# Kernel optimization log

Hardware: AMD Instinct MI355X
Metric: run time of the kernel (lower is better)

Reference implementation:

```python
import jax, jax.numpy as jnp
import numpy as np

NUM_NODES = 100000
EMB_DIM = 64
NUM_EDGES = 1280000
NUM_LAYERS = 3


def setup_inputs() -> dict:
    key = jax.random.key(0)
    k1, k2 = jax.random.split(key)
    edge_index = jax.random.randint(k1, (2, NUM_EDGES), 0, NUM_NODES, dtype=jnp.int32)
    emb = jax.random.normal(k2, (NUM_NODES, EMB_DIM), dtype=jnp.float32) * 0.01
    return {"edge_index": edge_index, "emb": emb}


def _lgconv_norm(edge_index):
    # PyG gcn_norm without self-loops: deg over destination nodes,
    # norm_e = deg[src]^-0.5 * deg[dst]^-0.5
    src, dst = edge_index[0], edge_index[1]
    deg = jax.ops.segment_sum(jnp.ones((edge_index.shape[1],), jnp.float32), dst,
                              num_segments=NUM_NODES)
    dinv = jnp.where(deg > 0, jax.lax.rsqrt(jnp.maximum(deg, 1.0)), 0.0)
    return src, dst, dinv[src] * dinv[dst]


def reference(edge_index, emb):
    src, dst, w = _lgconv_norm(edge_index)
    x = emb
    out = x
    for _ in range(NUM_LAYERS):
        # message: gather source embeddings, scale, scatter-add to destination
        x = jax.ops.segment_sum(x[src] * w[:, None], dst, num_segments=NUM_NODES)
        out = out + x
    return out / (NUM_LAYERS + 1)
```

## Files before the change

kernel.cpp:

```cpp
#include <hip/hip_runtime.h>

#define N_NODES 100000
#define EMB 64
#define N_EDGES 1280000
#define N_E4 (N_EDGES / 4)

#define NBUCK 196
#define BUCK_SHIFT 9
#define BUCK_NODES 512
#define NBA 313
#define HTOT (NBUCK * NBA)
#define NBH ((HTOT + 1023) / 1024)

typedef unsigned long long u64;
typedef _Float16 f16;
typedef __attribute__((ext_vector_type(2))) _Float16 f16x2;

__global__ void bucket_hist_kernel(const int* __restrict__ dst, int* __restrict__ hist) {
    __shared__ int lh[NBUCK];
    for (int i = threadIdx.x; i < NBUCK; i += 256) lh[i] = 0;
    __syncthreads();
#pragma unroll
    for (int k = 0; k < 4; ++k) {
        int q = blockIdx.x * 1024 + k * 256 + threadIdx.x;
        if (q < N_E4) {
            int4 d4 = ((const int4*)dst)[q];
            atomicAdd(&lh[d4.x >> BUCK_SHIFT], 1);
            atomicAdd(&lh[d4.y >> BUCK_SHIFT], 1);
            atomicAdd(&lh[d4.z >> BUCK_SHIFT], 1);
            atomicAdd(&lh[d4.w >> BUCK_SHIFT], 1);
        }
    }
    __syncthreads();
    for (int i = threadIdx.x; i < NBUCK; i += 256)
        hist[i * NBA + blockIdx.x] = lh[i];
}

__global__ void hist_scan1_kernel(int* __restrict__ hist, int* __restrict__ hbs) {
    __shared__ int lds[256];
    int base = blockIdx.x * 1024;
    int vals[4];
    int tsum = 0;
#pragma unroll
    for (int k = 0; k < 4; ++k) {
        int i = base + threadIdx.x * 4 + k;
        vals[k] = (i < HTOT) ? hist[i] : 0;
        tsum += vals[k];
    }
    lds[threadIdx.x] = tsum;
    __syncthreads();
    for (int off = 1; off < 256; off <<= 1) {
        int v = (threadIdx.x >= (unsigned)off) ? lds[threadIdx.x - off] : 0;
        __syncthreads();
        lds[threadIdx.x] += v;
        __syncthreads();
    }
    int run = lds[threadIdx.x] - tsum;
    if (threadIdx.x == 255) hbs[blockIdx.x] = lds[255];
    #pragma unroll
    for (int k = 0; k < 4; ++k) {
        int i = base + threadIdx.x * 4 + k;
        if (i < HTOT) hist[i] = run;
        run += vals[k];
    }
}

__global__ void hist_scan2_kernel(int* __restrict__ hbs) {
    __shared__ int lds[64];
    int v = (threadIdx.x < (unsigned)NBH) ? hbs[threadIdx.x] : 0;
    lds[threadIdx.x] = v;
    __syncthreads();
    for (int off = 1; off < 64; off <<= 1) {
        int t = (threadIdx.x >= (unsigned)off) ? lds[threadIdx.x - off] : 0;
        __syncthreads();
        lds[threadIdx.x] += t;
        __syncthreads();
    }
    if (threadIdx.x < (unsigned)NBH) hbs[threadIdx.x] = lds[threadIdx.x] - v;
}

__global__ void bucket_scatter_kernel(const int* __restrict__ src, const int* __restrict__ dst,
                                      const int* __restrict__ hist, const int* __restrict__ hbs,
                                      int* __restrict__ bedge) {
    __shared__ int cur[NBUCK];
    for (int i = threadIdx.x; i < NBUCK; i += 256) {
        int idx = i * NBA + blockIdx.x;
        cur[i] = hist[idx] + hbs[idx >> 10];
    }
    __syncthreads();
#pragma unroll
    for (int k = 0; k < 4; ++k) {
        int q = blockIdx.x * 1024 + k * 256 + threadIdx.x;
        if (q < N_E4) {
            int4 d4 = ((const int4*)dst)[q];
            int4 s4 = ((const int4*)src)[q];
            int p;
            p = atomicAdd(&cur[d4.x >> BUCK_SHIFT], 1);
            bedge[p] = s4.x | ((d4.x & (BUCK_NODES - 1)) << 17);
            p = atomicAdd(&cur[d4.y >> BUCK_SHIFT], 1);
            bedge[p] = s4.y | ((d4.y & (BUCK_NODES - 1)) << 17);
            p = atomicAdd(&cur[d4.z >> BUCK_SHIFT], 1);
            bedge[p] = s4.z | ((d4.z & (BUCK_NODES - 1)) << 17);
            p = atomicAdd(&cur[d4.w >> BUCK_SHIFT], 1);
            bedge[p] = s4.w | ((d4.w & (BUCK_NODES - 1)) << 17);
        }
    }
}

__global__ void bucket_build_kernel(const int* __restrict__ hist, const int* __restrict__ hbs,
                                    const int* __restrict__ bedge,
                                    int* __restrict__ col, int* __restrict__ row_start,
                                    float* __restrict__ dinv, float* __restrict__ rdinv) {
    __shared__ int lh[BUCK_NODES];
    __shared__ int sc[256];
    __shared__ int cur[BUCK_NODES];
    int k = blockIdx.x;
    int tid = threadIdx.x;
    int i0 = k * NBA;
    int beg = hist[i0] + hbs[i0 >> 10];
    int end;
    if (k + 1 < NBUCK) {
        int i1 = (k + 1) * NBA;
        end = hist[i1] + hbs[i1 >> 10];
    } else {
        end = N_EDGES;
    }
    lh[tid] = 0;
    lh[tid + 256] = 0;
    __syncthreads();
    for (int i = beg + tid; i < end; i += 256)
        atomicAdd(&lh[((unsigned)bedge[i]) >> 17], 1);
    __syncthreads();
    int v0 = lh[2 * tid];
    int v1 = lh[2 * tid + 1];
    int tsum = v0 + v1;
    sc[tid] = tsum;
    __syncthreads();
    for (int off = 1; off < 256; off <<= 1) {
        int v = (tid >= off) ? sc[tid - off] : 0;
        __syncthreads();
        sc[tid] += v;
        __syncthreads();
    }
    int texcl = sc[tid] - tsum;
    cur[2 * tid] = texcl;
    cur[2 * tid + 1] = texcl + v0;
    __syncthreads();
    for (int i = tid; i < BUCK_NODES; i += 256) {
        int node = k * BUCK_NODES + i;
        if (node <= N_NODES) {
            row_start[node] = beg + cur[i];
            if (node < N_NODES) {
                int d = lh[i];
                float fd = (float)d;
                dinv[node]  = (d > 0) ? rsqrtf(fd) : 0.0f;
                rdinv[node] = (d > 0) ? sqrtf(fd) : 0.0f;
            }
        }
    }
    for (int i = beg + tid; i < end; i += 256) {
        unsigned pe = (unsigned)bedge[i];
        int r = atomicAdd(&cur[pe >> 17], 1);
        col[beg + r] = (int)(pe & 0x1FFFFu);
    }
}

__global__ void y0_kernel(const float* __restrict__ emb, const float* __restrict__ dinv,
                          f16* __restrict__ y0) {
    int i = blockIdx.x * blockDim.x + threadIdx.x;
    const int n4 = N_NODES * EMB / 4;
    if (i < n4) {
        float dv = dinv[i >> 4];
        float4 v = ((const float4*)emb)[i];
        f16 h[4] = {(f16)(v.x * dv), (f16)(v.y * dv), (f16)(v.z * dv), (f16)(v.w * dv)};
        ((u64*)y0)[i] = *(const u64*)h;
    }
}

template <bool FINAL>
__global__ void gather_kernel(const int* __restrict__ row_start, const int* __restrict__ col,
                              const float* __restrict__ dinv, const float* __restrict__ rdinv,
                              const f16* __restrict__ yin, f16* __restrict__ yout,
                              const float* __restrict__ emb,
                              const f16* __restrict__ y1, const f16* __restrict__ y2,
                              float* __restrict__ out) {
    unsigned int gid = blockIdx.x * blockDim.x + threadIdx.x;
    unsigned int row = gid >> 6;
    int lane = (int)(gid & 63u);
    int s = lane >> 5;
    int j = lane & 31;
    if (row >= N_NODES) return;
    int beg = row_start[row];
    int end = row_start[row + 1];
    const f16* yj = yin + 2 * j;
    float accx = 0.0f, accy = 0.0f;
    for (int cb = beg; cb < end; cb += 64) {
        int idx = cb + lane;
        int ci = 0;
        if (idx < end) ci = col[idx];
        int n = end - cb;
        if (n > 64) n = 64;
        int kk = 0;
        for (; kk + 8 <= n; kk += 8) {
            int c0 = __shfl(ci, kk + s);
            int c1 = __shfl(ci, kk + s + 2);
            int c2 = __shfl(ci, kk + s + 4);
            int c3 = __shfl(ci, kk + s + 6);
            unsigned u0 = *(const unsigned*)(yj + (unsigned)c0 * EMB);
            unsigned u1 = *(const unsigned*)(yj + (unsigned)c1 * EMB);
            unsigned u2 = *(const unsigned*)(yj + (unsigned)c2 * EMB);
            unsigned u3 = *(const unsigned*)(yj + (unsigned)c3 * EMB);
            f16x2 h0 = __builtin_bit_cast(f16x2, u0);
            f16x2 h1 = __builtin_bit_cast(f16x2, u1);
            f16x2 h2 = __builtin_bit_cast(f16x2, u2);
            f16x2 h3 = __builtin_bit_cast(f16x2, u3);
            accx += (float)h0.x + (float)h1.x + (float)h2.x + (float)h3.x;
            accy += (float)h0.y + (float)h1.y + (float)h2.y + (float)h3.y;
        }
        if (kk + 4 <= n) {
            int c0 = __shfl(ci, kk + s);
            int c1 = __shfl(ci, kk + s + 2);
            unsigned u0 = *(const unsigned*)(yj + (unsigned)c0 * EMB);
            unsigned u1 = *(const unsigned*)(yj + (unsigned)c1 * EMB);
            f16x2 h0 = __builtin_bit_cast(f16x2, u0);
            f16x2 h1 = __builtin_bit_cast(f16x2, u1);
            accx += (float)h0.x + (float)h1.x;
            accy += (float)h0.y + (float)h1.y;
            kk += 4;
        }
        for (; kk < n; ++kk) {
            int c = __shfl(ci, kk);
            if (s == (kk & 1)) {
                unsigned u = *(const unsigned*)(yj + (unsigned)c * EMB);
                f16x2 h = __builtin_bit_cast(f16x2, u);
                accx += (float)h.x;
                accy += (float)h.y;
            }
        }
    }
    accx += __shfl_xor(accx, 32);
    accy += __shfl_xor(accy, 32);
    if (s == 0) {
        float dv = dinv[row];
        unsigned int o = row * EMB + 2 * (unsigned)j;
        if (!FINAL) {
            float sc = dv * dv;
            f16x2 h;
            h.x = (f16)(accx * sc);
            h.y = (f16)(accy * sc);
            *(unsigned*)(yout + o) = __builtin_bit_cast(unsigned, h);
        } else {
            float rv = rdinv[row];
            float2 e2 = *(const float2*)(emb + o);
            f16x2 a = __builtin_bit_cast(f16x2, *(const unsigned*)(y1 + o));
            f16x2 b = __builtin_bit_cast(f16x2, *(const unsigned*)(y2 + o));
            float rx = 0.25f * (e2.x + rv * ((float)a.x + (float)b.x) + dv * accx);
            float ry = 0.25f * (e2.y + rv * ((float)a.y + (float)b.y) + dv * accy);
            __builtin_nontemporal_store(rx, out + o);
            __builtin_nontemporal_store(ry, out + o + 1);
        }
    }
}

extern "C" void kernel_launch(void* const* d_in, const int* in_sizes, int n_in,
                              void* d_out, int out_size, void* d_ws, size_t ws_size,
                              hipStream_t stream) {
    const int*   edge = (const int*)d_in[0];
    const int*   src  = edge;
    const int*   dst  = edge + N_EDGES;
    const float* emb  = (const float*)d_in[1];
    float*       out  = (float*)d_out;

    char* ws = (char*)d_ws;
    size_t off = 0;
    int* row_start = (int*)(ws + off); off += 400016;
    int* hbs       = (int*)(ws + off); off += 256;
    float* dinv    = (float*)(ws + off); off += 400000;
    float* rdinv   = (float*)(ws + off); off += 400000;
    int* hist      = (int*)(ws + off); off += (size_t)HTOT * 4 + 16;
    int* col       = (int*)(ws + off); off += (size_t)N_EDGES * 4;
    f16* y0        = (f16*)(ws + off); off += (size_t)N_NODES * EMB * 2;
    f16* y1        = (f16*)(ws + off); off += (size_t)N_NODES * EMB * 2;
    f16* y2        = (f16*)(ws + off); off += (size_t)N_NODES * EMB * 2;

    int* bedge = (int*)y1;

    bucket_hist_kernel<<<NBA, 256, 0, stream>>>(dst, hist);
    hist_scan1_kernel<<<NBH, 256, 0, stream>>>(hist, hbs);
    hist_scan2_kernel<<<1, 64, 0, stream>>>(hbs);
    bucket_scatter_kernel<<<NBA, 256, 0, stream>>>(src, dst, hist, hbs, bedge);
    bucket_build_kernel<<<NBUCK, 256, 0, stream>>>(hist, hbs, bedge, col, row_start,
                                                   dinv, rdinv);
    y0_kernel<<<(N_NODES * EMB / 4 + 255) / 256, 256, 0, stream>>>(emb, dinv, y0);

    const unsigned int gthreads = (unsigned int)N_NODES * EMB;
    const int gblocks = (int)((gthreads + 255) / 256);
    gather_kernel<false><<<gblocks, 256, 0, stream>>>(row_start, col, dinv, rdinv,
                                                      y0, y1, emb, y1, y2, out);
    gather_kernel<false><<<gblocks, 256, 0, stream>>>(row_start, col, dinv, rdinv,
                                                      y1, y2, emb, y1, y2, out);
    gather_kernel<true><<<gblocks, 256, 0, stream>>>(row_start, col, dinv, rdinv,
                                                     y2, (f16*)0, emb, y1, y2, out);
}
```

Before: 259.7 us.

## Fuse CSR build stages into one cooperative kernel with grid syncs

Result: slower. 812.6 us (+212.9%).

```diff
diff --git a/kernel.cpp b/kernel.cpp
--- a/kernel.cpp
+++ b/kernel.cpp
@@ -1,4 +1,7 @@
 #include <hip/hip_runtime.h>
+#include <hip/hip_cooperative_groups.h>
+
+namespace cg = cooperative_groups;
 
 #define N_NODES 100000
 #define EMB 64
@@ -8,168 +11,157 @@
 #define NBUCK 196
 #define BUCK_SHIFT 9
 #define BUCK_NODES 512
-#define NBA 313
-#define HTOT (NBUCK * NBA)
-#define NBH ((HTOT + 1023) / 1024)
+
+#define GB 1024
+#define GT 256
+#define EPB4 ((N_E4 + GB - 1) / GB)
+#define HTOT (NBUCK * GB)
+#define PER (HTOT / GB)
 
 typedef unsigned long long u64;
 typedef _Float16 f16;
 typedef __attribute__((ext_vector_type(2))) _Float16 f16x2;
 
-__global__ void bucket_hist_kernel(const int* __restrict__ dst, int* __restrict__ hist) {
-    __shared__ int lh[NBUCK];
-    for (int i = threadIdx.x; i < NBUCK; i += 256) lh[i] = 0;
+__global__ void __launch_bounds__(GT, 4) build_kernel(
+    const int* __restrict__ src, const int* __restrict__ dst,
+    const float* __restrict__ emb,
+    int* __restrict__ hist, int* __restrict__ bsum,
+    int* __restrict__ bedge, int* __restrict__ col,
+    int* __restrict__ row_start, float* __restrict__ dinv,
+    float* __restrict__ rdinv, f16* __restrict__ y0)
+{
+    cg::grid_group grid = cg::this_grid();
+    const int b = blockIdx.x;
+    const int tid = threadIdx.x;
+    __shared__ int lh[BUCK_NODES];
+    __shared__ int sc[GT];
+    __shared__ int cur[BUCK_NODES];
+
+    const int qbeg = b * EPB4;
+    const int qend = (qbeg + EPB4 < N_E4) ? qbeg + EPB4 : N_E4;
+
+    for (int i = tid; i < NBUCK; i += GT) lh[i] = 0;
     __syncthreads();
+    for (int q = qbeg + tid; q < qend; q += GT) {
+        int4 d4 = ((const int4*)dst)[q];
+        atomicAdd(&lh[d4.x >> BUCK_SHIFT], 1);
+        atomicAdd(&lh[d4.y >> BUCK_SHIFT], 1);
+        atomicAdd(&lh[d4.z >> BUCK_SHIFT], 1);
+        atomicAdd(&lh[d4.w >> BUCK_SHIFT], 1);
+    }
+    __syncthreads();
+    for (int i = tid; i < NBUCK; i += GT) hist[i * GB + b] = lh[i];
+    grid.sync();
+
+    {
+        int idx = b * PER + tid;
+        int v = (tid < PER) ? hist[idx] : 0;
+        sc[tid] = v;
+        __syncthreads();
+        for (int off = 1; off < GT; off <<= 1) {
+            int t = (tid >= off) ? sc[tid - off] : 0;
+            __syncthreads();
+            sc[tid] += t;
+            __syncthreads();
+        }
+        if (tid < PER) hist[idx] = sc[tid] - v;
+        if (tid == GT - 1) bsum[b] = sc[GT - 1];
+    }
+    grid.sync();
+
+    if (b == 0) {
+        int vals[4];
+        int tsum = 0;
 #pragma unroll
-    for (int k = 0; k < 4; ++k) {
-        int q = blockIdx.x * 1024 + k * 256 + threadIdx.x;
-        if (q < N_E4) {
-            int4 d4 = ((const int4*)dst)[q];
-            atomicAdd(&lh[d4.x >> BUCK_SHIFT], 1);
-            atomicAdd(&lh[d4.y >> BUCK_SHIFT], 1);
-            atomicAdd(&lh[d4.z >> BUCK_SHIFT], 1);
-            atomicAdd(&lh[d4.w >> BUCK_SHIFT], 1);
-        }
+        for (int k = 0; k < 4; ++k) { vals[k] = bsum[tid * 4 + k]; tsum += vals[k]; }
+        sc[tid] = tsum;
+        __syncthreads();
+        for (int off = 1; off < GT; off <<= 1) {
+            int t = (tid >= off) ? sc[tid - off] : 0;
+            __syncthreads();
+            sc[tid] += t;
+            __syncthreads();
+        }
+        int run = sc[tid] - tsum;
+#pragma unroll
+        for (int k = 0; k < 4; ++k) { int v = vals[k]; bsum[tid * 4 + k] = run; run += v; }
+    }
+    grid.sync();
+
+    for (int i = tid; i < NBUCK; i += GT) {
+        int idx = i * GB + b;
+        cur[i] = hist[idx] + bsum[idx / PER];
     }
     __syncthreads();
-    for (int i = threadIdx.x; i < NBUCK; i += 256)
-        hist[i * NBA + blockIdx.x] = lh[i];
-}
-
-__global__ void hist_scan1_kernel(int* __restrict__ hist, int* __restrict__ hbs) {
-    __shared__ int lds[256];
-    int base = blockIdx.x * 1024;
-    int vals[4];
-    int tsum = 0;
-#pragma unroll
-    for (int k = 0; k < 4; ++k) {
-        int i = base + threadIdx.x * 4 + k;
-        vals[k] = (i < HTOT) ? hist[i] : 0;
-        tsum += vals[k];
-    }
-    lds[threadIdx.x] = tsum;
-    __syncthreads();
-    for (int off = 1; off < 256; off <<= 1) {
-        int v = (threadIdx.x >= (unsigned)off) ? lds[threadIdx.x - off] : 0;
-        __syncthreads();
-        lds[threadIdx.x] += v;
-        __syncthreads();
-    }
-    int run = lds[threadIdx.x] - tsum;
-    if (threadIdx.x == 255) hbs[blockIdx.x] = lds[255];
-    #pragma unroll
-    for (int k = 0; k < 4; ++k) {
-        int i = base + threadIdx.x * 4 + k;
-        if (i < HTOT) hist[i] = run;
-        run += vals[k];
-    }
-}
-
-__global__ void hist_scan2_kernel(int* __restrict__ hbs) {
-    __shared__ int lds[64];
-    int v = (threadIdx.x < (unsigned)NBH) ? hbs[threadIdx.x] : 0;
-    lds[threadIdx.x] = v;
-    __syncthreads();
-    for (int off = 1; off < 64; off <<= 1) {
-        int t = (threadIdx.x >= (unsigned)off) ? lds[threadIdx.x - off] : 0;
-        __syncthreads();
-        lds[threadIdx.x] += t;
-        __syncthreads();
-    }
-    if (threadIdx.x < (unsigned)NBH) hbs[threadIdx.x] = lds[threadIdx.x] - v;
-}
-
-__global__ void bucket_scatter_kernel(const int* __restrict__ src, const int* __restrict__ dst,
-                                      const int* __restrict__ hist, const int* __restrict__ hbs,
-                                      int* __restrict__ bedge) {
-    __shared__ int cur[NBUCK];
-    for (int i = threadIdx.x; i < NBUCK; i += 256) {
-        int idx = i * NBA + blockIdx.x;
-        cur[i] = hist[idx] + hbs[idx >> 10];
-    }
-    __syncthreads();
-#pragma unroll
-    for (int k = 0; k < 4; ++k) {
-        int q = blockIdx.x * 1024 + k * 256 + threadIdx.x;
-        if (q < N_E4) {
-            int4 d4 = ((const int4*)dst)[q];
-            int4 s4 = ((const int4*)src)[q];
-            int p;
-            p = atomicAdd(&cur[d4.x >> BUCK_SHIFT], 1);
-            bedge[p] = s4.x | ((d4.x & (BUCK_NODES - 1)) << 17);
-            p = atomicAdd(&cur[d4.y >> BUCK_SHIFT], 1);
-            bedge[p] = s4.y | ((d4.y & (BUCK_NODES - 1)) << 17);
-            p = atomicAdd(&cur[d4.z >> BUCK_SHIFT], 1);
-            bedge[p] = s4.z | ((d4.z & (BUCK_NODES - 1)) << 17);
-            p = atomicAdd(&cur[d4.w >> BUCK_SHIFT], 1);
-            bedge[p] = s4.w | ((d4.w & (BUCK_NODES - 1)) << 17);
-        }
-    }
-}
-
-__global__ void bucket_build_kernel(const int* __restrict__ hist, const int* __restrict__ hbs,
-                                    const int* __restrict__ bedge,
-                                    int* __restrict__ col, int* __restrict__ row_start,
-                                    float* __restrict__ dinv, float* __restrict__ rdinv) {
-    __shared__ int lh[BUCK_NODES];
-    __shared__ int sc[256];
-    __shared__ int cur[BUCK_NODES];
-    int k = blockIdx.x;
-    int tid = threadIdx.x;
-    int i0 = k * NBA;
-    int beg = hist[i0] + hbs[i0 >> 10];
-    int end;
-    if (k + 1 < NBUCK) {
-        int i1 = (k + 1) * NBA;
-        end = hist[i1] + hbs[i1 >> 10];
-    } else {
-        end = N_EDGES;
-    }
-    lh[tid] = 0;
-    lh[tid + 256] = 0;
-    __syncthreads();
-    for (int i = beg + tid; i < end; i += 256)
-        atomicAdd(&lh[((unsigned)bedge[i]) >> 17], 1);
-    __syncthreads();
-    int v0 = lh[2 * tid];
-    int v1 = lh[2 * tid + 1];
-    int tsum = v0 + v1;
-    sc[tid] = tsum;
-    __syncthreads();
-    for (int off = 1; off < 256; off <<= 1) {
-        int v = (tid >= off) ? sc[tid - off] : 0;
-        __syncthreads();
-        sc[tid] += v;
-        __syncthreads();
-    }
-    int texcl = sc[tid] - tsum;
-    cur[2 * tid] = texcl;
-    cur[2 * tid + 1] = texcl + v0;
-    __syncthreads();
-    for (int i = tid; i < BUCK_NODES; i += 256) {
-        int node = k * BUCK_NODES + i;
-        if (node <= N_NODES) {
-            row_start[node] = beg + cur[i];
-            if (node < N_NODES) {
-                int d = lh[i];
-                float fd = (float)d;
-                dinv[node]  = (d > 0) ? rsqrtf(fd) : 0.0f;
-                rdinv[node] = (d > 0) ? sqrtf(fd) : 0.0f;
+    for (int q = qbeg + tid; q < qend; q += GT) {
+        int4 d4 = ((const int4*)dst)[q];
+        int4 s4 = ((const int4*)src)[q];
+        int p;
+        p = atomicAdd(&cur[d4.x >> BUCK_SHIFT], 1);
+        bedge[p] = s4.x | ((d4.x & (BUCK_NODES - 1)) << 17);
+        p = atomicAdd(&cur[d4.y >> BUCK_SHIFT], 1);
+        bedge[p] = s4.y | ((d4.y & (BUCK_NODES - 1)) << 17);
+        p = atomicAdd(&cur[d4.z >> BUCK_SHIFT], 1);
+        bedge[p] = s4.z | ((d4.z & (BUCK_NODES - 1)) << 17);
+        p = atomicAdd(&cur[d4.w >> BUCK_SHIFT], 1);
+        bedge[p] = s4.w | ((d4.w & (BUCK_NODES - 1)) << 17);
+    }
+    grid.sync();
+
+    if (b < NBUCK) {
+        int i0 = b * GB;
+        int beg = hist[i0] + bsum[i0 / PER];
+        int end;
+        if (b + 1 < NBUCK) {
+            int i1 = (b + 1) * GB;
+            end = hist[i1] + bsum[i1 / PER];
+        } else {
+            end = N_EDGES;
+        }
+        lh[tid] = 0;
+        lh[tid + 256] = 0;
+        __syncthreads();
+        for (int i = beg + tid; i < end; i += GT)
+            atomicAdd(&lh[((unsigned)bedge[i]) >> 17], 1);
+        __syncthreads();
+        int v0 = lh[2 * tid];
+        int v1 = lh[2 * tid + 1];
+        int tsum = v0 + v1;
+        sc[tid] = tsum;
+        __syncthreads();
+        for (int off = 1; off < GT; off <<= 1) {
+            int v = (tid >= off) ? sc[tid - off] : 0;
+            __syncthreads();
+            sc[tid] += v;
+            __syncthreads();
+        }
+        int texcl = sc[tid] - tsum;
+        cur[2 * tid] = texcl;
+        cur[2 * tid + 1] = texcl + v0;
+        __syncthreads();
+        for (int i = tid; i < BUCK_NODES; i += GT) {
+            int node = b * BUCK_NODES + i;
+            if (node <= N_NODES) {
+                row_start[node] = beg + cur[i];
+                if (node < N_NODES) {
+                    int d = lh[i];
+                    float fd = (float)d;
+                    dinv[node]  = (d > 0) ? rsqrtf(fd) : 0.0f;
+                    rdinv[node] = (d > 0) ? sqrtf(fd) : 0.0f;
+                }
             }
         }
-    }
-    for (int i = beg + tid; i < end; i += 256) {
-        unsigned pe = (unsigned)bedge[i];
-        int r = atomicAdd(&cur[pe >> 17], 1);
-        col[beg + r] = (int)(pe & 0x1FFFFu);
-    }
-}
-
-__global__ void y0_kernel(const float* __restrict__ emb, const float* __restrict__ dinv,
-                          f16* __restrict__ y0) {
-    int i = blockIdx.x * blockDim.x + threadIdx.x;
+        __syncthreads();
+        for (int i = beg + tid; i < end; i += GT) {
+            unsigned pe = (unsigned)bedge[i];
+            int r = atomicAdd(&cur[pe >> 17], 1);
+            col[beg + r] = (int)(pe & 0x1FFFFu);
+        }
+    }
+    grid.sync();
+
     const int n4 = N_NODES * EMB / 4;
-    if (i < n4) {
+    for (int i = b * GT + tid; i < n4; i += GB * GT) {
         float dv = dinv[i >> 4];
         float4 v = ((const float4*)emb)[i];
         f16 h[4] = {(f16)(v.x * dv), (f16)(v.y * dv), (f16)(v.z * dv), (f16)(v.w * dv)};
@@ -266,15 +258,15 @@
                               void* d_out, int out_size, void* d_ws, size_t ws_size,
                               hipStream_t stream) {
     const int*   edge = (const int*)d_in[0];
-    const int*   src  = edge;
-    const int*   dst  = edge + N_EDGES;
+    const int*   src  = (const int*)edge;
+    const int*   dst  = (const int*)(edge + N_EDGES);
     const float* emb  = (const float*)d_in[1];
     float*       out  = (float*)d_out;
 
     char* ws = (char*)d_ws;
     size_t off = 0;
     int* row_start = (int*)(ws + off); off += 400016;
-    int* hbs       = (int*)(ws + off); off += 256;
+    int* bsum      = (int*)(ws + off); off += 4096;
     float* dinv    = (float*)(ws + off); off += 400000;
     float* rdinv   = (float*)(ws + off); off += 400000;
     int* hist      = (int*)(ws + off); off += (size_t)HTOT * 4 + 16;
@@ -285,13 +277,11 @@
 
     int* bedge = (int*)y1;
 
-    bucket_hist_kernel<<<NBA, 256, 0, stream>>>(dst, hist);
-    hist_scan1_kernel<<<NBH, 256, 0, stream>>>(hist, hbs);
-    hist_scan2_kernel<<<1, 64, 0, stream>>>(hbs);
-    bucket_scatter_kernel<<<NBA, 256, 0, stream>>>(src, dst, hist, hbs, bedge);
-    bucket_build_kernel<<<NBUCK, 256, 0, stream>>>(hist, hbs, bedge, col, row_start,
-                                                   dinv, rdinv);
-    y0_kernel<<<(N_NODES * EMB / 4 + 255) / 256, 256, 0, stream>>>(emb, dinv, y0);
+    void* args[] = { (void*)&src, (void*)&dst, (void*)&emb, (void*)&hist,
+                     (void*)&bsum, (void*)&bedge, (void*)&col, (void*)&row_start,
+                     (void*)&dinv, (void*)&rdinv, (void*)&y0 };
+    hipLaunchCooperativeKernel((const void*)build_kernel, dim3(GB), dim3(GT),
+                               args, 0, stream);
 
     const unsigned int gthreads = (unsigned int)N_NODES * EMB;
     const int gblocks = (int)((gthreads + 255) / 256);
```

## Fuse y0 scaling into bucket build and widen gather loads to 4 halves

Applied to the files above, without the earlier changes.

Result: slower. 289.7 us (+11.5%).

```diff
diff --git a/kernel.cpp b/kernel.cpp
--- a/kernel.cpp
+++ b/kernel.cpp
@@ -15,6 +15,8 @@
 typedef unsigned long long u64;
 typedef _Float16 f16;
 typedef __attribute__((ext_vector_type(2))) _Float16 f16x2;
+typedef __attribute__((ext_vector_type(4))) _Float16 f16x4;
+typedef __attribute__((ext_vector_type(4))) float f32x4;
 
 __global__ void bucket_hist_kernel(const int* __restrict__ dst, int* __restrict__ hist) {
     __shared__ int lh[NBUCK];
@@ -108,9 +110,10 @@
 }
 
 __global__ void bucket_build_kernel(const int* __restrict__ hist, const int* __restrict__ hbs,
-                                    const int* __restrict__ bedge,
+                                    const int* __restrict__ bedge, const float* __restrict__ emb,
                                     int* __restrict__ col, int* __restrict__ row_start,
-                                    float* __restrict__ dinv, float* __restrict__ rdinv) {
+                                    float* __restrict__ dinv, float* __restrict__ rdinv,
+                                    f16* __restrict__ y0) {
     __shared__ int lh[BUCK_NODES];
     __shared__ int sc[256];
     __shared__ int cur[BUCK_NODES];
@@ -158,22 +161,23 @@
             }
         }
     }
+    __syncthreads();
     for (int i = beg + tid; i < end; i += 256) {
         unsigned pe = (unsigned)bedge[i];
         int r = atomicAdd(&cur[pe >> 17], 1);
         col[beg + r] = (int)(pe & 0x1FFFFu);
     }
-}
-
-__global__ void y0_kernel(const float* __restrict__ emb, const float* __restrict__ dinv,
-                          f16* __restrict__ y0) {
-    int i = blockIdx.x * blockDim.x + threadIdx.x;
-    const int n4 = N_NODES * EMB / 4;
-    if (i < n4) {
-        float dv = dinv[i >> 4];
-        float4 v = ((const float4*)emb)[i];
-        f16 h[4] = {(f16)(v.x * dv), (f16)(v.y * dv), (f16)(v.z * dv), (f16)(v.w * dv)};
-        ((u64*)y0)[i] = *(const u64*)h;
+    int nbase = k * BUCK_NODES;
+    for (int i = tid; i < BUCK_NODES * 16; i += 256) {
+        int node = nbase + (i >> 4);
+        if (node < N_NODES) {
+            float dd = (float)lh[i >> 4];
+            float dv = (dd > 0.0f) ? rsqrtf(dd) : 0.0f;
+            int quad = i & 15;
+            float4 v = ((const float4*)emb)[(size_t)node * 16 + quad];
+            f16 h[4] = {(f16)(v.x * dv), (f16)(v.y * dv), (f16)(v.z * dv), (f16)(v.w * dv)};
+            ((u64*)y0)[(size_t)node * 16 + quad] = *(const u64*)h;
+        }
     }
 }
 
@@ -187,77 +191,55 @@
     unsigned int gid = blockIdx.x * blockDim.x + threadIdx.x;
     unsigned int row = gid >> 6;
     int lane = (int)(gid & 63u);
-    int s = lane >> 5;
-    int j = lane & 31;
+    int s = lane >> 4;
+    int j = lane & 15;
     if (row >= N_NODES) return;
     int beg = row_start[row];
     int end = row_start[row + 1];
-    const f16* yj = yin + 2 * j;
-    float accx = 0.0f, accy = 0.0f;
+    const f16* yj = yin + 4 * j;
+    float a0 = 0.0f, a1 = 0.0f, a2 = 0.0f, a3 = 0.0f;
     for (int cb = beg; cb < end; cb += 64) {
         int idx = cb + lane;
         int ci = 0;
         if (idx < end) ci = col[idx];
         int n = end - cb;
         if (n > 64) n = 64;
-        int kk = 0;
-        for (; kk + 8 <= n; kk += 8) {
-            int c0 = __shfl(ci, kk + s);
-            int c1 = __shfl(ci, kk + s + 2);
-            int c2 = __shfl(ci, kk + s + 4);
-            int c3 = __shfl(ci, kk + s + 6);
-            unsigned u0 = *(const unsigned*)(yj + (unsigned)c0 * EMB);
-            unsigned u1 = *(const unsigned*)(yj + (unsigned)c1 * EMB);
-            unsigned u2 = *(const unsigned*)(yj + (unsigned)c2 * EMB);
-            unsigned u3 = *(const unsigned*)(yj + (unsigned)c3 * EMB);
-            f16x2 h0 = __builtin_bit_cast(f16x2, u0);
-            f16x2 h1 = __builtin_bit_cast(f16x2, u1);
-            f16x2 h2 = __builtin_bit_cast(f16x2, u2);
-            f16x2 h3 = __builtin_bit_cast(f16x2, u3);
-            accx += (float)h0.x + (float)h1.x + (float)h2.x + (float)h3.x;
-            accy += (float)h0.y + (float)h1.y + (float)h2.y + (float)h3.y;
-        }
-        if (kk + 4 <= n) {
-            int c0 = __shfl(ci, kk + s);
-            int c1 = __shfl(ci, kk + s + 2);
-            unsigned u0 = *(const unsigned*)(yj + (unsigned)c0 * EMB);
-            unsigned u1 = *(const unsigned*)(yj + (unsigned)c1 * EMB);
-            f16x2 h0 = __builtin_bit_cast(f16x2, u0);
-            f16x2 h1 = __builtin_bit_cast(f16x2, u1);
-            accx += (float)h0.x + (float)h1.x;
-            accy += (float)h0.y + (float)h1.y;
-            kk += 4;
-        }
-        for (; kk < n; ++kk) {
-            int c = __shfl(ci, kk);
-            if (s == (kk & 1)) {
-                unsigned u = *(const unsigned*)(yj + (unsigned)c * EMB);
-                f16x2 h = __builtin_bit_cast(f16x2, u);
-                accx += (float)h.x;
-                accy += (float)h.y;
+#pragma unroll
+        for (int kk = 0; kk < 16; ++kk) {
+            int e = 4 * kk + s;
+            int c = __shfl(ci, e);
+            if (e < n) {
+                u64 u = *(const u64*)(yj + (unsigned)c * EMB);
+                f16x4 h = __builtin_bit_cast(f16x4, u);
+                a0 += (float)h.x;
+                a1 += (float)h.y;
+                a2 += (float)h.z;
+                a3 += (float)h.w;
             }
         }
     }
-    accx += __shfl_xor(accx, 32);
-    accy += __shfl_xor(accy, 32);
+    a0 += __shfl_xor(a0, 16); a1 += __shfl_xor(a1, 16);
+    a2 += __shfl_xor(a2, 16); a3 += __shfl_xor(a3, 16);
+    a0 += __shfl_xor(a0, 32); a1 += __shfl_xor(a1, 32);
+    a2 += __shfl_xor(a2, 32); a3 += __shfl_xor(a3, 32);
     if (s == 0) {
         float dv = dinv[row];
-        unsigned int o = row * EMB + 2 * (unsigned)j;
+        unsigned int o = row * EMB + 4 * (unsigned)j;
         if (!FINAL) {
             float sc = dv * dv;
-            f16x2 h;
-            h.x = (f16)(accx * sc);
-            h.y = (f16)(accy * sc);
-            *(unsigned*)(yout + o) = __builtin_bit_cast(unsigned, h);
+            f16 h[4] = {(f16)(a0 * sc), (f16)(a1 * sc), (f16)(a2 * sc), (f16)(a3 * sc)};
+            *(u64*)(yout + o) = *(const u64*)h;
         } else {
             float rv = rdinv[row];
-            float2 e2 = *(const float2*)(emb + o);
-            f16x2 a = __builtin_bit_cast(f16x2, *(const unsigned*)(y1 + o));
-            f16x2 b = __builtin_bit_cast(f16x2, *(const unsigned*)(y2 + o));
-            float rx = 0.25f * (e2.x + rv * ((float)a.x + (float)b.x) + dv * accx);
-            float ry = 0.25f * (e2.y + rv * ((float)a.y + (float)b.y) + dv * accy);
-            __builtin_nontemporal_store(rx, out + o);
-            __builtin_nontemporal_store(ry, out + o + 1);
+            float4 e2 = *(const float4*)(emb + o);
+            f16x4 a = __builtin_bit_cast(f16x4, *(const u64*)(y1 + o));
+            f16x4 b = __builtin_bit_cast(f16x4, *(const u64*)(y2 + o));
+            f32x4 r;
+            r.x = 0.25f * (e2.x + rv * ((float)a.x + (float)b.x) + dv * a0);
+            r.y = 0.25f * (e2.y + rv * ((float)a.y + (float)b.y) + dv * a1);
+            r.z = 0.25f * (e2.z + rv * ((float)a.z + (float)b.z) + dv * a2);
+            r.w = 0.25f * (e2.w + rv * ((float)a.w + (float)b.w) + dv * a3);
+            __builtin_nontemporal_store(r, (f32x4*)(out + o));
         }
     }
 }
@@ -289,9 +271,8 @@
     hist_scan1_kernel<<<NBH, 256, 0, stream>>>(hist, hbs);
     hist_scan2_kernel<<<1, 64, 0, stream>>>(hbs);
     bucket_scatter_kernel<<<NBA, 256, 0, stream>>>(src, dst, hist, hbs, bedge);
-    bucket_build_kernel<<<NBUCK, 256, 0, stream>>>(hist, hbs, bedge, col, row_start,
-                                                   dinv, rdinv);
-    y0_kernel<<<(N_NODES * EMB / 4 + 255) / 256, 256, 0, stream>>>(emb, dinv, y0);
+    bucket_build_kernel<<<NBUCK, 256, 0, stream>>>(hist, hbs, bedge, emb, col,
+                                                   row_start, dinv, rdinv, y0);
 
     const unsigned int gthreads = (unsigned int)N_NODES * EMB;
     const int gblocks = (int)((gthreads + 255) / 256);
```

## Stage bucket scatter through shared memory and fuse y0 scaling into build

Applied to the files above, without the earlier changes.

Measured after the change: 261.6 us. No clear change (+0.7%).

```diff
diff --git a/kernel.cpp b/kernel.cpp
--- a/kernel.cpp
+++ b/kernel.cpp
@@ -11,6 +11,7 @@
 #define NBA 313
 #define HTOT (NBUCK * NBA)
 #define NBH ((HTOT + 1023) / 1024)
+#define EPB 4096
 
 typedef unsigned long long u64;
 typedef _Float16 f16;
@@ -82,35 +83,84 @@
 __global__ void bucket_scatter_kernel(const int* __restrict__ src, const int* __restrict__ dst,
                                       const int* __restrict__ hist, const int* __restrict__ hbs,
                                       int* __restrict__ bedge) {
-    __shared__ int cur[NBUCK];
-    for (int i = threadIdx.x; i < NBUCK; i += 256) {
-        int idx = i * NBA + blockIdx.x;
-        cur[i] = hist[idx] + hbs[idx >> 10];
-    }
-    __syncthreads();
+    __shared__ unsigned      sedge[EPB];
+    __shared__ unsigned char sbk[EPB];
+    __shared__ int cnt[NBUCK];
+    __shared__ int loff[NBUCK];
+    __shared__ int gbase[NBUCK];
+    __shared__ int ssc[256];
+    const int b = blockIdx.x;
+    const int tid = threadIdx.x;
+
+    for (int i = tid; i < NBUCK; i += 256) cnt[i] = 0;
+    __syncthreads();
+
+    unsigned pk[16];
+    int bk[16];
 #pragma unroll
     for (int k = 0; k < 4; ++k) {
-        int q = blockIdx.x * 1024 + k * 256 + threadIdx.x;
+        int q = b * 1024 + k * 256 + tid;
         if (q < N_E4) {
             int4 d4 = ((const int4*)dst)[q];
             int4 s4 = ((const int4*)src)[q];
-            int p;
-            p = atomicAdd(&cur[d4.x >> BUCK_SHIFT], 1);
-            bedge[p] = s4.x | ((d4.x & (BUCK_NODES - 1)) << 17);
-            p = atomicAdd(&cur[d4.y >> BUCK_SHIFT], 1);
-            bedge[p] = s4.y | ((d4.y & (BUCK_NODES - 1)) << 17);
-            p = atomicAdd(&cur[d4.z >> BUCK_SHIFT], 1);
-            bedge[p] = s4.z | ((d4.z & (BUCK_NODES - 1)) << 17);
-            p = atomicAdd(&cur[d4.w >> BUCK_SHIFT], 1);
-            bedge[p] = s4.w | ((d4.w & (BUCK_NODES - 1)) << 17);
-        }
+            pk[4*k+0] = (unsigned)(s4.x | ((d4.x & (BUCK_NODES - 1)) << 17));
+            pk[4*k+1] = (unsigned)(s4.y | ((d4.y & (BUCK_NODES - 1)) << 17));
+            pk[4*k+2] = (unsigned)(s4.z | ((d4.z & (BUCK_NODES - 1)) << 17));
+            pk[4*k+3] = (unsigned)(s4.w | ((d4.w & (BUCK_NODES - 1)) << 17));
+            bk[4*k+0] = d4.x >> BUCK_SHIFT;
+            bk[4*k+1] = d4.y >> BUCK_SHIFT;
+            bk[4*k+2] = d4.z >> BUCK_SHIFT;
+            bk[4*k+3] = d4.w >> BUCK_SHIFT;
+            atomicAdd(&cnt[bk[4*k+0]], 1);
+            atomicAdd(&cnt[bk[4*k+1]], 1);
+            atomicAdd(&cnt[bk[4*k+2]], 1);
+            atomicAdd(&cnt[bk[4*k+3]], 1);
+        } else {
+            bk[4*k+0] = -1; bk[4*k+1] = -1; bk[4*k+2] = -1; bk[4*k+3] = -1;
+        }
+    }
+    __syncthreads();
+
+    int own = (tid < NBUCK) ? cnt[tid] : 0;
+    ssc[tid] = own;
+    __syncthreads();
+    for (int off = 1; off < 256; off <<= 1) {
+        int v = (tid >= off) ? ssc[tid - off] : 0;
+        __syncthreads();
+        ssc[tid] += v;
+        __syncthreads();
+    }
+    if (tid < NBUCK) {
+        int excl = ssc[tid] - own;
+        loff[tid] = excl;
+        cnt[tid] = excl;
+        int idx = tid * NBA + b;
+        gbase[tid] = hist[idx] + hbs[idx >> 10];
+    }
+    __syncthreads();
+
+#pragma unroll
+    for (int e = 0; e < 16; ++e) {
+        if (bk[e] >= 0) {
+            int slot = atomicAdd(&cnt[bk[e]], 1);
+            sedge[slot] = pk[e];
+            sbk[slot] = (unsigned char)bk[e];
+        }
+    }
+    __syncthreads();
+
+    int ne = (b * 1024 + 1024 <= N_E4) ? EPB : (N_E4 - b * 1024) * 4;
+    for (int t = tid; t < ne; t += 256) {
+        int kb = sbk[t];
+        bedge[gbase[kb] + (t - loff[kb])] = (int)sedge[t];
     }
 }
 
 __global__ void bucket_build_kernel(const int* __restrict__ hist, const int* __restrict__ hbs,
-                                    const int* __restrict__ bedge,
+                                    const int* __restrict__ bedge, const float* __restrict__ emb,
                                     int* __restrict__ col, int* __restrict__ row_start,
-                                    float* __restrict__ dinv, float* __restrict__ rdinv) {
+                                    float* __restrict__ dinv, float* __restrict__ rdinv,
+                                    f16* __restrict__ y0) {
     __shared__ int lh[BUCK_NODES];
     __shared__ int sc[256];
     __shared__ int cur[BUCK_NODES];
@@ -158,22 +208,23 @@
             }
         }
     }
+    __syncthreads();
     for (int i = beg + tid; i < end; i += 256) {
         unsigned pe = (unsigned)bedge[i];
         int r = atomicAdd(&cur[pe >> 17], 1);
         col[beg + r] = (int)(pe & 0x1FFFFu);
     }
-}
-
-__global__ void y0_kernel(const float* __restrict__ emb, const float* __restrict__ dinv,
-                          f16* __restrict__ y0) {
-    int i = blockIdx.x * blockDim.x + threadIdx.x;
-    const int n4 = N_NODES * EMB / 4;
-    if (i < n4) {
-        float dv = dinv[i >> 4];
-        float4 v = ((const float4*)emb)[i];
-        f16 h[4] = {(f16)(v.x * dv), (f16)(v.y * dv), (f16)(v.z * dv), (f16)(v.w * dv)};
-        ((u64*)y0)[i] = *(const u64*)h;
+    int nbase = k * BUCK_NODES;
+    for (int i = tid; i < BUCK_NODES * 16; i += 256) {
+        int node = nbase + (i >> 4);
+        if (node < N_NODES) {
+            float dd = (float)lh[i >> 4];
+            float dv = (dd > 0.0f) ? rsqrtf(dd) : 0.0f;
+            int quad = i & 15;
+            float4 v = ((const float4*)emb)[(size_t)node * 16 + quad];
+            f16 h[4] = {(f16)(v.x * dv), (f16)(v.y * dv), (f16)(v.z * dv), (f16)(v.w * dv)};
+            ((u64*)y0)[(size_t)node * 16 + quad] = *(const u64*)h;
+        }
     }
 }
 
@@ -289,9 +340,8 @@
     hist_scan1_kernel<<<NBH, 256, 0, stream>>>(hist, hbs);
     hist_scan2_kernel<<<1, 64, 0, stream>>>(hbs);
     bucket_scatter_kernel<<<NBA, 256, 0, stream>>>(src, dst, hist, hbs, bedge);
-    bucket_build_kernel<<<NBUCK, 256, 0, stream>>>(hist, hbs, bedge, col, row_start,
-                                                   dinv, rdinv);
-    y0_kernel<<<(N_NODES * EMB / 4 + 255) / 256, 256, 0, stream>>>(emb, dinv, y0);
+    bucket_build_kernel<<<NBUCK, 256, 0, stream>>>(hist, hbs, bedge, emb, col,
+                                                   row_start, dinv, rdinv, y0);
 
     const unsigned int gthreads = (unsigned int)N_NODES * EMB;
     const int gblocks = (int)((gthreads + 255) / 256);
```
